# Performance work log

Hardware: AMD Instinct MI355X
Metric: run time of the kernel (lower is better)

Reference implementation:

```python
import jax, jax.numpy as jnp
import numpy as np

B, N, E = 32, 2048, 1048576  # 32 uniform graphs of 2048 nodes, avg degree 16
BN = B * N
KS = (1024, 512, 256)  # TopKPooling ratio=0.5 -> ceil(0.5*n) per layer (uniform graphs -> static)


def _mlp2(x, w1, b1, w2, b2):
    # nn.Sequential(Linear, ReLU, Linear)
    return jnp.maximum(x @ w1 + b1, 0.0) @ w2 + b2


def _forward(x, edge_attr, node_w1, node_b1, node_w2, node_b2,
             edge_w1, edge_b1, edge_w2, edge_b2,
             eff_in_w, eff_in_b, eff_h_w, eff_h_b, eff_out_w, eff_out_b,
             upd_in_w, upd_in_b, upd_h_w, upd_h_b, upd_out_w, upd_out_b,
             pool_w, edge_index):
    relu = lambda t: jnp.maximum(t, 0.0)
    src, dst = edge_index[0], edge_index[1]  # PyG: x_j = h[src], x_i = h[dst], aggregate at dst
    h = _mlp2(x, node_w1, node_b1, node_w2, node_b2)          # [BN, F] node embedding
    e = _mlp2(edge_attr, edge_w1, edge_b1, edge_w2, edge_b2)  # [E, F]  edge embedding
    node_mask = jnp.ones((BN,), bool)
    edge_mask = jnp.ones((E,), bool)
    for i in range(3):
        # --- DPIGNNLayer: gather-concat-MLP(+edge_attr) message, scatter-mean aggregate ---
        m = jnp.concatenate([h[dst], h[src]], axis=-1)        # [E, 2F] = cat(x_i, x_j)
        m = relu(m @ eff_in_w[i] + eff_in_b[i])
        m = relu(m @ eff_h_w[i] + eff_h_b[i])
        m = relu(m @ eff_out_w[i] + eff_out_b[i] + e)
        em = edge_mask.astype(h.dtype)[:, None]
        agg = jax.ops.segment_sum(m * em, dst, num_segments=BN)
        cnt = jax.ops.segment_sum(em, dst, num_segments=BN)
        mean = agg / jnp.maximum(cnt, 1.0)                    # mean aggr (0 where no edges)
        u = jnp.concatenate([mean, h], axis=-1)
        u = relu(u @ upd_in_w[i] + upd_in_b[i])
        u = relu(u @ upd_h_w[i] + upd_h_b[i])
        _ = relu(u @ upd_out_w[i] + upd_out_b[i] + h)  # dead compute: source update() returns x
        # --- TopKPooling(ratio=0.5), masked form (uniform graph sizes -> static k) ---
        w = pool_w[i]
        score = jnp.tanh((h @ w) / jnp.linalg.norm(w))        # [BN]
        masked = jnp.where(node_mask, score, -jnp.inf).reshape(B, N)
        _, idx = jax.lax.top_k(masked, KS[i])                 # [B, k]
        sel = jnp.zeros((B, N), bool).at[jnp.arange(B)[:, None], idx].set(True).reshape(-1)
        node_mask = sel
        h = jnp.where(node_mask[:, None], h * score[:, None], 0.0)
        edge_mask = edge_mask & node_mask[src] & node_mask[dst]  # filter_adj equivalent
    # global_mean_pool over surviving nodes per graph
    nm = node_mask.astype(h.dtype)[:, None]
    sums = (h * nm).reshape(B, N, -1).sum(axis=1)
    cnts = nm.reshape(B, N, 1).sum(axis=1)
    return sums / jnp.maximum(cnts, 1.0)  # [B, F]


def setup_inputs() -> dict:
    key = jax.random.key(0)
    ks = iter(jax.random.split(key, 40))
    F, ND, ED = 128, 16, 8
    s = 0.05
    W = lambda shape: jax.random.normal(next(ks), shape, jnp.float32) * s
    zb = lambda shape: jnp.zeros(shape, jnp.float32)
    e_per = E // B
    base = (jnp.arange(E) // e_per) * N  # graph offset per edge
    src = jax.random.randint(next(ks), (E,), 0, N) + base
    dst = jax.random.randint(next(ks), (E,), 0, N) + base
    return {
        'x': jax.random.normal(next(ks), (BN, ND), jnp.float32),
        'edge_attr': jax.random.normal(next(ks), (E, ED), jnp.float32),
        'node_w1': W((ND, F)), 'node_b1': zb((F,)),
        'node_w2': W((F, F)), 'node_b2': zb((F,)),
        'edge_w1': W((ED, F)), 'edge_b1': zb((F,)),
        'edge_w2': W((F, F)), 'edge_b2': zb((F,)),
        'eff_in_w': W((3, 2 * F, F)), 'eff_in_b': zb((3, F)),
        'eff_h_w': W((3, F, F)), 'eff_h_b': zb((3, F)),
        'eff_out_w': W((3, F, F)), 'eff_out_b': zb((3, F)),
        'upd_in_w': W((3, 2 * F, F)), 'upd_in_b': zb((3, F)),
        'upd_h_w': W((3, F, F)), 'upd_h_b': zb((3, F)),
        'upd_out_w': W((3, F, F)), 'upd_out_b': zb((3, F)),
        'pool_w': W((3, F)),
        'edge_index': jnp.stack([src, dst]),
    }


def reference(x, edge_attr, node_w1, node_b1, node_w2, node_b2,
              edge_w1, edge_b1, edge_w2, edge_b2,
              eff_in_w, eff_in_b, eff_h_w, eff_h_b, eff_out_w, eff_out_b,
              upd_in_w, upd_in_b, upd_h_w, upd_h_b, upd_out_w, upd_out_b,
              pool_w, edge_index):
    return _forward(x, edge_attr, node_w1, node_b1, node_w2, node_b2,
                    edge_w1, edge_b1, edge_w2, edge_b2,
                    eff_in_w, eff_in_b, eff_h_w, eff_h_b, eff_out_w, eff_out_b,
                    upd_in_w, upd_in_b, upd_h_w, upd_h_b, upd_out_w, upd_out_b,
                    pool_w, edge_index)
```

## Files before the change

kernel.cpp:

```cpp
#include <hip/hip_runtime.h>
#include <hip/hip_bf16.h>


#define NPG    2048
#define NGRAPH 32
#define HP     2112
#define HPAD(b) ((b) + ((b) >> 5))

__global__ __launch_bounds__(256) void k1_fused(
    const float* __restrict__ x,
    const float* __restrict__ W1,
    const float* __restrict__ b1,
    const float* __restrict__ W2,
    const float* __restrict__ b2,
    const float* __restrict__ pw,
    float4* __restrict__ d4)
{
    __shared__ float4 sW1v[512];
    __shared__ float4 sb1v[32];
    __shared__ __align__(16) float swn[384];
    __shared__ __align__(16) float sv[384];
    __shared__ float sc[4];
    __shared__ float snorm[3];
    int t = threadIdx.x;
    int lane = t & 63, wv = t >> 6;

    for (int i = t; i < 512; i += 256) sW1v[i] = ((const float4*)W1)[i];
    if (t < 32) sb1v[t] = ((const float4*)b1)[t];
    if (wv < 3) {
        float w0 = pw[wv * 128 + lane];
        float w1 = pw[wv * 128 + 64 + lane];
        float p = w0 * w0 + w1 * w1;
        #pragma unroll
        for (int s = 32; s; s >>= 1) p += __shfl_xor(p, s);
        if (lane == 0) snorm[wv] = sqrtf(p);
    }
    __syncthreads();
    for (int i = t; i < 384; i += 256) swn[i] = pw[i] / snorm[i >> 7];
    __syncthreads();
    for (int task = t; task < 387; task += 256) {
        int k = task / 129, j = task % 129;
        const float4* r4 = (const float4*)((j < 128) ? (W2 + j * 128) : b2);
        const float* wn = swn + k * 128;
        float p0 = 0.f, p1 = 0.f, p2 = 0.f, p3 = 0.f;
        #pragma unroll 8
        for (int q = 0; q < 32; ++q) {
            float4 w = r4[q];
            p0 = fmaf(w.x, wn[4 * q + 0], p0);
            p1 = fmaf(w.y, wn[4 * q + 1], p1);
            p2 = fmaf(w.z, wn[4 * q + 2], p2);
            p3 = fmaf(w.w, wn[4 * q + 3], p3);
        }
        float p = (p0 + p1) + (p2 + p3);
        if (j < 128) sv[k * 128 + j] = p;
        else sc[k] = p;
    }
    __syncthreads();

    int n = blockIdx.x * 256 + t;
    const float4* xr = (const float4*)(x + (size_t)n * 16);
    float4 xa = xr[0], xb = xr[1], xc = xr[2], xd = xr[3];
    float xs[16] = {xa.x, xa.y, xa.z, xa.w, xb.x, xb.y, xb.z, xb.w,
                    xc.x, xc.y, xc.z, xc.w, xd.x, xd.y, xd.z, xd.w};
    const float4* sv4 = (const float4*)sv;
    float dd0 = sc[0], dd1 = sc[1], dd2 = sc[2];
    #pragma unroll 4
    for (int fq = 0; fq < 32; ++fq) {
        float4 a4 = sb1v[fq];
        #pragma unroll
        for (int j = 0; j < 16; ++j) {
            float4 w = sW1v[j * 32 + fq];
            a4.x = fmaf(xs[j], w.x, a4.x);
            a4.y = fmaf(xs[j], w.y, a4.y);
            a4.z = fmaf(xs[j], w.z, a4.z);
            a4.w = fmaf(xs[j], w.w, a4.w);
        }
        a4.x = fmaxf(a4.x, 0.f); a4.y = fmaxf(a4.y, 0.f);
        a4.z = fmaxf(a4.z, 0.f); a4.w = fmaxf(a4.w, 0.f);
        float4 v0 = sv4[fq], v1 = sv4[32 + fq], v2 = sv4[64 + fq];
        dd0 = fmaf(a4.x, v0.x, fmaf(a4.y, v0.y, fmaf(a4.z, v0.z, fmaf(a4.w, v0.w, dd0))));
        dd1 = fmaf(a4.x, v1.x, fmaf(a4.y, v1.y, fmaf(a4.z, v1.z, fmaf(a4.w, v1.w, dd1))));
        dd2 = fmaf(a4.x, v2.x, fmaf(a4.y, v2.y, fmaf(a4.z, v2.z, fmaf(a4.w, v2.w, dd2))));
    }
    d4[n] = make_float4(dd0, dd1, dd2, 0.f);
}

__global__ __launch_bounds__(1024, 1) void k2_cascade(
    const float* __restrict__ x,
    const float* __restrict__ W1,
    const float* __restrict__ b1,
    const float* __restrict__ W2,
    const float* __restrict__ b2,
    const float4* __restrict__ d4,
    float* __restrict__ out)
{
    __shared__ float d0A[NPG], d1A[NPG], d2A[NPG];
    __shared__ unsigned long long sKey[NPG];
    __shared__ unsigned int hist[2][HP];
    __shared__ int   idxB[1024];
    __shared__ float cscB[1024], d1B[1024], d2B[1024];
    __shared__ int   idxA2[512];
    __shared__ float cscA2[512], d2A2[512];
    __shared__ float sW1[2048], sb1[128];
    __shared__ float Spart[1024], Svec[128], red4[4];
    __shared__ unsigned long long sPrefix;
    __shared__ int sNeed, sDone, sCnt;

    int t = threadIdx.x, g = blockIdx.x;
    int lane = t & 63, wv = t >> 6;

    for (int n = t; n < NPG; n += 1024) {
        float4 dd = d4[g * NPG + n];
        d0A[n] = dd.x; d1A[n] = dd.y; d2A[n] = dd.z;
    }
    for (int i = t; i < 2048; i += 1024) sW1[i] = W1[i];
    if (t < 128) sb1[t] = b1[t];
    for (int i = t; i < 2 * HP; i += 1024) ((unsigned int*)hist)[i] = 0u;
    __syncthreads();

    int curN = NPG;
    for (int r = 0; r < 3; ++r) {
        int kk = 1024 >> r;
        const float* dIn   = (r == 0) ? d0A : (r == 1) ? d1B : d2A2;
        const float* cscIn = (r == 0) ? (const float*)0 : (r == 1) ? cscB : cscA2;
        const int*   idxIn = (r == 0) ? (const int*)0 : (r == 1) ? idxB : idxA2;
        int*   idxOut = (r == 1) ? idxA2 : idxB;
        float* cscOut = (r == 1) ? cscA2 : cscB;

        if (t == 0) { sPrefix = 0ull; sNeed = kk; sDone = 0; sCnt = 0; }
        for (int m = t; m < curN; m += 1024) {
            float ci = cscIn ? cscIn[m] : 1.f;
            int   ni = idxIn ? idxIn[m] : m;
            float z = ci * dIn[m];
            unsigned int bb = __float_as_uint(z);
            unsigned int mo = (bb & 0x80000000u) ? ~bb : (bb | 0x80000000u);
            unsigned long long kv = ((unsigned long long)mo << 11)
                                  | (unsigned long long)(unsigned int)(2047 - ni);
            sKey[m] = kv;
            atomicAdd(&hist[0][HPAD((unsigned int)(kv >> 33) & 2047u)], 1u);
        }
        __syncthreads();

        int lastBuf = 0;
        for (int pass = 0; pass < 4; ++pass) {
            int buf = pass & 1;
            int shift = 33 - 11 * pass;
            lastBuf = buf;
            if (pass > 0) {
                unsigned long long pref = sPrefix;
                for (int m = t; m < curN; m += 1024) {
                    unsigned long long kv = sKey[m];
                    if ((kv >> (shift + 11)) == (pref >> (shift + 11)))
                        atomicAdd(&hist[buf][HPAD((unsigned int)(kv >> shift) & 2047u)], 1u);
                }
                __syncthreads();
            }
            if (wv == 0) {
                unsigned long long pref = sPrefix;
                unsigned int need = (unsigned int)sNeed;
                unsigned int h[32], tl = 0;
                #pragma unroll
                for (int b = 0; b < 32; ++b) {
                    h[b] = hist[buf][HPAD(32u * t + b)];
                    tl += h[b];
                }
                unsigned int s = tl;
                #pragma unroll
                for (int d = 1; d < 64; d <<= 1) {
                    unsigned int v = __shfl_down(s, d);
                    if (t + d < 64) s += v;
                }
                unsigned int above = s - tl;
                if (above < need && above + tl >= need) {
                    unsigned int cum = above;
                    #pragma unroll
                    for (int b = 31; b >= 0; --b) {
                        cum += h[b];
                        if (cum >= need) {
                            int nn = (int)(need - (cum - h[b]));
                            sNeed = nn;
                            sPrefix = pref |
                                ((unsigned long long)(unsigned int)(32 * t + b) << shift);
                            sDone = (nn == (int)h[b]) || (pass == 3);
                            break;
                        }
                    }
                }
            } else if (pass > 0) {
                for (int i = t - 64; i < HP; i += 960) hist[buf ^ 1][i] = 0u;
            }
            __syncthreads();
            if (sDone) break;
        }
        unsigned long long thr = sPrefix;

        for (int i = t; i < HP; i += 1024) hist[lastBuf][i] = 0u;
        for (int m = t; m < curN; m += 1024) {
            unsigned long long kv = sKey[m];
            bool pred = (kv >= thr);
            unsigned long long mask = __ballot(pred);
            if (mask) {
                int leader = __ffsll((long long)mask) - 1;
                int cnt = __popcll(mask);
                int base = 0;
                if (lane == leader) base = atomicAdd(&sCnt, cnt);
                base = __shfl(base, leader);
                if (pred) {
                    int rank = __popcll(mask & ((1ull << lane) - 1ull));
                    int pos = base + rank;
                    float ci = cscIn ? cscIn[m] : 1.f;
                    int   ni = idxIn ? idxIn[m] : m;
                    float z = ci * dIn[m];
                    idxOut[pos] = ni;
                    cscOut[pos] = ci * tanhf(z);
                    if (r == 0)      { d1B[pos] = d1A[m]; d2B[pos] = d2A[m]; }
                    else if (r == 1) { d2A2[pos] = d2B[m]; }
                }
            }
        }
        __syncthreads();
        curN = kk;
    }

    {
        int f = t & 127, grp = t >> 7;
        float Sacc = 0.f;
        for (int it = grp; it < 256; it += 8) {
            int n = idxB[it];
            float cn = cscB[it];
            const float4* xr = (const float4*)(x + (size_t)(g * NPG + n) * 16);
            float4 xa = xr[0], xb = xr[1], xc = xr[2], xd = xr[3];
            float acc = sb1[f];
            acc = fmaf(xa.x, sW1[0 * 128 + f], acc);
            acc = fmaf(xa.y, sW1[1 * 128 + f], acc);
            acc = fmaf(xa.z, sW1[2 * 128 + f], acc);
            acc = fmaf(xa.w, sW1[3 * 128 + f], acc);
            acc = fmaf(xb.x, sW1[4 * 128 + f], acc);
            acc = fmaf(xb.y, sW1[5 * 128 + f], acc);
            acc = fmaf(xb.z, sW1[6 * 128 + f], acc);
            acc = fmaf(xb.w, sW1[7 * 128 + f], acc);
            acc = fmaf(xc.x, sW1[8 * 128 + f], acc);
            acc = fmaf(xc.y, sW1[9 * 128 + f], acc);
            acc = fmaf(xc.z, sW1[10 * 128 + f], acc);
            acc = fmaf(xc.w, sW1[11 * 128 + f], acc);
            acc = fmaf(xd.x, sW1[12 * 128 + f], acc);
            acc = fmaf(xd.y, sW1[13 * 128 + f], acc);
            acc = fmaf(xd.z, sW1[14 * 128 + f], acc);
            acc = fmaf(xd.w, sW1[15 * 128 + f], acc);
            Sacc += fmaxf(acc, 0.f) * cn;
        }
        Spart[t] = Sacc;
    }
    if (t < 256) {
        float cpart = cscB[t];
        #pragma unroll
        for (int s = 32; s; s >>= 1) cpart += __shfl_xor(cpart, s);
        if ((t & 63) == 0) red4[t >> 6] = cpart;
    }
    __syncthreads();
    if (t < 128) {
        float sv = 0.f;
        #pragma unroll
        for (int h = 0; h < 8; ++h) sv += Spart[h * 128 + t];
        Svec[t] = sv;
    }
    __syncthreads();
    if (t < 128) {
        float Csum = (red4[0] + red4[1]) + (red4[2] + red4[3]);
        float acc = Csum * b2[t];
        for (int j = 0; j < 128; ++j)
            acc = fmaf(Svec[j], W2[j * 128 + t], acc);
        out[g * 128 + t] = acc * (1.0f / 256.0f);
    }
}

extern "C" void kernel_launch(void* const* d_in, const int* in_sizes, int n_in,
                              void* d_out, int out_size, void* d_ws, size_t ws_size,
                              hipStream_t stream) {
    const float* x  = (const float*)d_in[0];
    const float* W1 = (const float*)d_in[2];
    const float* b1 = (const float*)d_in[3];
    const float* W2 = (const float*)d_in[4];
    const float* b2 = (const float*)d_in[5];
    const float* pw = (const float*)d_in[22];
    float* out = (float*)d_out;

    float4* d4 = (float4*)d_ws;

    k1_fused<<<256, 256, 0, stream>>>(x, W1, b1, W2, b2, pw, d4);
    k2_cascade<<<NGRAPH, 1024, 0, stream>>>(x, W1, b1, W2, b2, d4, out);
}
```

Before: 168.2 us.

## Trim LDS staging, decode scores from keys, split final W2 matvec

Measured after the change: 175.6 us. +4.4%, slower.

```diff
diff --git a/kernel.cpp b/kernel.cpp
--- a/kernel.cpp
+++ b/kernel.cpp
@@ -6,6 +6,15 @@
 #define NGRAPH 32
 #define HP     2112
 #define HPAD(b) ((b) + ((b) >> 5))
+
+__device__ __forceinline__ unsigned int mono_bits(float z) {
+    unsigned int bb = __float_as_uint(z);
+    return (bb & 0x80000000u) ? ~bb : (bb | 0x80000000u);
+}
+__device__ __forceinline__ float mono_decode(unsigned int mo) {
+    unsigned int bb = (mo & 0x80000000u) ? (mo & 0x7FFFFFFFu) : ~mo;
+    return __uint_as_float(bb);
+}
 
 __global__ __launch_bounds__(256) void k1_fused(
     const float* __restrict__ x,
@@ -16,8 +25,6 @@
     const float* __restrict__ pw,
     float4* __restrict__ d4)
 {
-    __shared__ float4 sW1v[512];
-    __shared__ float4 sb1v[32];
     __shared__ __align__(16) float swn[384];
     __shared__ __align__(16) float sv[384];
     __shared__ float sc[4];
@@ -25,8 +32,6 @@
     int t = threadIdx.x;
     int lane = t & 63, wv = t >> 6;
 
-    for (int i = t; i < 512; i += 256) sW1v[i] = ((const float4*)W1)[i];
-    if (t < 32) sb1v[t] = ((const float4*)b1)[t];
     if (wv < 3) {
         float w0 = pw[wv * 128 + lane];
         float w1 = pw[wv * 128 + 64 + lane];
@@ -57,6 +62,8 @@
     }
     __syncthreads();
 
+    const float4* W1v = (const float4*)W1;
+    const float4* b1v = (const float4*)b1;
     int n = blockIdx.x * 256 + t;
     const float4* xr = (const float4*)(x + (size_t)n * 16);
     float4 xa = xr[0], xb = xr[1], xc = xr[2], xd = xr[3];
@@ -66,10 +73,10 @@
     float dd0 = sc[0], dd1 = sc[1], dd2 = sc[2];
     #pragma unroll 4
     for (int fq = 0; fq < 32; ++fq) {
-        float4 a4 = sb1v[fq];
+        float4 a4 = b1v[fq];
         #pragma unroll
         for (int j = 0; j < 16; ++j) {
-            float4 w = sW1v[j * 32 + fq];
+            float4 w = W1v[j * 32 + fq];
             a4.x = fmaf(xs[j], w.x, a4.x);
             a4.y = fmaf(xs[j], w.y, a4.y);
             a4.z = fmaf(xs[j], w.z, a4.z);
@@ -94,8 +101,8 @@
     const float4* __restrict__ d4,
     float* __restrict__ out)
 {
-    __shared__ float d0A[NPG], d1A[NPG], d2A[NPG];
     __shared__ unsigned long long sKey[NPG];
+    __shared__ float d1A[NPG], d2A[NPG];
     __shared__ unsigned int hist[2][HP];
     __shared__ int   idxB[1024];
     __shared__ float cscB[1024], d1B[1024], d2B[1024];
@@ -108,38 +115,52 @@
 
     int t = threadIdx.x, g = blockIdx.x;
     int lane = t & 63, wv = t >> 6;
-
-    for (int n = t; n < NPG; n += 1024) {
-        float4 dd = d4[g * NPG + n];
-        d0A[n] = dd.x; d1A[n] = dd.y; d2A[n] = dd.z;
-    }
+    const float4* d4g = d4 + (size_t)g * NPG;
+
+    float4 e0 = d4g[t];
+    float4 e1 = d4g[t + 1024];
     for (int i = t; i < 2048; i += 1024) sW1[i] = W1[i];
     if (t < 128) sb1[t] = b1[t];
     for (int i = t; i < 2 * HP; i += 1024) ((unsigned int*)hist)[i] = 0u;
+    if (t == 0) { sPrefix = 0ull; sNeed = 1024; sDone = 0; sCnt = 0; }
+    __syncthreads();
+
+    {
+        unsigned long long kv0 = ((unsigned long long)mono_bits(e0.x) << 11)
+                               | (unsigned long long)(unsigned int)(2047 - t);
+        d1A[t] = e0.y; d2A[t] = e0.z;
+        sKey[t] = kv0;
+        atomicAdd(&hist[0][HPAD((unsigned int)(kv0 >> 33) & 2047u)], 1u);
+        int n1 = t + 1024;
+        unsigned long long kv1 = ((unsigned long long)mono_bits(e1.x) << 11)
+                               | (unsigned long long)(unsigned int)(2047 - n1);
+        d1A[n1] = e1.y; d2A[n1] = e1.z;
+        sKey[n1] = kv1;
+        atomicAdd(&hist[0][HPAD((unsigned int)(kv1 >> 33) & 2047u)], 1u);
+    }
     __syncthreads();
 
     int curN = NPG;
     for (int r = 0; r < 3; ++r) {
         int kk = 1024 >> r;
-        const float* dIn   = (r == 0) ? d0A : (r == 1) ? d1B : d2A2;
-        const float* cscIn = (r == 0) ? (const float*)0 : (r == 1) ? cscB : cscA2;
-        const int*   idxIn = (r == 0) ? (const int*)0 : (r == 1) ? idxB : idxA2;
+        const float* cscIn = (r == 1) ? cscB : cscA2;
         int*   idxOut = (r == 1) ? idxA2 : idxB;
         float* cscOut = (r == 1) ? cscA2 : cscB;
 
-        if (t == 0) { sPrefix = 0ull; sNeed = kk; sDone = 0; sCnt = 0; }
-        for (int m = t; m < curN; m += 1024) {
-            float ci = cscIn ? cscIn[m] : 1.f;
-            int   ni = idxIn ? idxIn[m] : m;
-            float z = ci * dIn[m];
-            unsigned int bb = __float_as_uint(z);
-            unsigned int mo = (bb & 0x80000000u) ? ~bb : (bb | 0x80000000u);
-            unsigned long long kv = ((unsigned long long)mo << 11)
-                                  | (unsigned long long)(unsigned int)(2047 - ni);
-            sKey[m] = kv;
-            atomicAdd(&hist[0][HPAD((unsigned int)(kv >> 33) & 2047u)], 1u);
-        }
-        __syncthreads();
+        if (r > 0) {
+            const float* dIn   = (r == 1) ? d1B : d2A2;
+            const int*   idxIn = (r == 1) ? idxB : idxA2;
+            if (t == 0) { sPrefix = 0ull; sNeed = kk; sDone = 0; sCnt = 0; }
+            __syncthreads();
+            for (int m = t; m < curN; m += 1024) {
+                float z = cscIn[m] * dIn[m];
+                unsigned long long kv = ((unsigned long long)mono_bits(z) << 11)
+                    | (unsigned long long)(unsigned int)(2047 - idxIn[m]);
+                sKey[m] = kv;
+                atomicAdd(&hist[0][HPAD((unsigned int)(kv >> 33) & 2047u)], 1u);
+            }
+            __syncthreads();
+        }
 
         int lastBuf = 0;
         for (int pass = 0; pass < 4; ++pass) {
@@ -208,13 +229,16 @@
                 if (pred) {
                     int rank = __popcll(mask & ((1ull << lane) - 1ull));
                     int pos = base + rank;
-                    float ci = cscIn ? cscIn[m] : 1.f;
-                    int   ni = idxIn ? idxIn[m] : m;
-                    float z = ci * dIn[m];
+                    float z = mono_decode((unsigned int)(kv >> 11));
+                    int ni = 2047 - (int)((unsigned int)kv & 2047u);
                     idxOut[pos] = ni;
-                    cscOut[pos] = ci * tanhf(z);
-                    if (r == 0)      { d1B[pos] = d1A[m]; d2B[pos] = d2A[m]; }
-                    else if (r == 1) { d2A2[pos] = d2B[m]; }
+                    if (r == 0) {
+                        cscOut[pos] = tanhf(z);
+                        d1B[pos] = d1A[m]; d2B[pos] = d2A[m];
+                    } else {
+                        cscOut[pos] = cscIn[m] * tanhf(z);
+                        if (r == 1) d2A2[pos] = d2B[m];
+                    }
                 }
             }
         }
@@ -225,6 +249,7 @@
     {
         int f = t & 127, grp = t >> 7;
         float Sacc = 0.f;
+        #pragma unroll 2
         for (int it = grp; it < 256; it += 8) {
             int n = idxB[it];
             float cn = cscB[it];
@@ -265,11 +290,20 @@
         Svec[t] = sv;
     }
     __syncthreads();
+    {
+        int f = t & 127, jc = t >> 7;
+        float part = 0.f;
+        #pragma unroll
+        for (int j = 16 * jc; j < 16 * jc + 16; ++j)
+            part = fmaf(Svec[j], W2[j * 128 + f], part);
+        Spart[t] = part;
+    }
+    __syncthreads();
     if (t < 128) {
         float Csum = (red4[0] + red4[1]) + (red4[2] + red4[3]);
         float acc = Csum * b2[t];
-        for (int j = 0; j < 128; ++j)
-            acc = fmaf(Svec[j], W2[j * 128 + t], acc);
+        #pragma unroll
+        for (int h = 0; h < 8; ++h) acc += Spart[h * 128 + t];
         out[g * 128 + t] = acc * (1.0f / 256.0f);
     }
 }
```
